# Performance work log

Hardware: AMD Instinct MI355X
Metric: run time of the kernel (lower is better)

The kernel has to match this reference:

```python
import jax, jax.numpy as jnp
import numpy as np

B, L, H, DK, DV, D, FC, NL = 8, 2016, 4, 32, 32, 256, 64, 3
EPS = 1e-5
SCALE = 1.0 / np.sqrt(float(D))  # module uses 1/sqrt(d_model), not 1/sqrt(dim_k)


def _ln(x, g, b):
    m = jnp.mean(x, axis=-1, keepdims=True)
    v = jnp.mean((x - m) ** 2, axis=-1, keepdims=True)
    return (x - m) * jax.lax.rsqrt(v + EPS) * g + b


def setup_inputs() -> dict:
    key = jax.random.key(0)
    ks = iter(jax.random.split(key, 32))

    def lin(k, shape, fan_in):
        # torch nn.Linear default: U(-1/sqrt(fan_in), 1/sqrt(fan_in))
        lim = 1.0 / np.sqrt(float(fan_in))
        return jax.random.uniform(k, shape, minval=-lim, maxval=lim, dtype=jnp.float32)

    inp = {
        'x': jax.random.normal(next(ks), (B, L, 2), dtype=jnp.float32),
        'in_w': lin(next(ks), (2, D), 2),
        'in_b': lin(next(ks), (D,), 2),
        'qw': lin(next(ks), (NL, D, H * DK), D),
        'qb': lin(next(ks), (NL, H * DK), D),
        'kw': lin(next(ks), (NL, D, H * DK), D),
        'kb': lin(next(ks), (NL, H * DK), D),
        'vw': lin(next(ks), (NL, D, H * DV), D),
        'vb': lin(next(ks), (NL, H * DV), D),
        'ow': lin(next(ks), (NL, H * DV, D), H * DV),
        'ob': lin(next(ks), (NL, D), H * DV),
        'f1w': lin(next(ks), (NL, D, FC), D),
        'f1b': lin(next(ks), (NL, FC), D),
        'f2w': lin(next(ks), (NL, FC, D), FC),
        'f2b': lin(next(ks), (NL, D), FC),
        'n1g': jnp.ones((NL, D), jnp.float32),
        'n1b': jnp.zeros((NL, D), jnp.float32),
        'n2g': jnp.ones((NL, D), jnp.float32),
        'n2b': jnp.zeros((NL, D), jnp.float32),
        'o1w': lin(next(ks), (D, D), D),
        'o1b': lin(next(ks), (D,), D),
        'o2w': lin(next(ks), (D, 2), D),
        'o2b': lin(next(ks), (2,), D),
    }
    return inp


def reference(x, in_w, in_b, qw, qb, kw, kb, vw, vb, ow, ob,
              f1w, f1b, f2w, f2b, n1g, n1b, n2g, n2b,
              o1w, o1b, o2w, o2b):
    h = x @ in_w + in_b  # (B, L, D)
    attns = []
    for i in range(NL):
        Q = (h @ qw[i] + qb[i]).reshape(B, L, H, DK)
        K = (h @ kw[i] + kb[i]).reshape(B, L, H, DK)
        V = (h @ vw[i] + vb[i]).reshape(B, L, H, DV)
        scores = jnp.einsum('blhe,bshe->bhls', Q, K) * SCALE  # (B,H,L,L)
        scores = jax.nn.softmax(scores, axis=-1)
        o = jnp.einsum('bhls,bshd->blhd', scores, V).reshape(B, L, H * DV)
        h = _ln(h + (o @ ow[i] + ob[i]), n1g[i], n1b[i])  # dropout is identity at eval
        ff = jax.nn.relu(h @ f1w[i] + f1b[i]) @ f2w[i] + f2b[i]
        h = _ln(h + ff, n2g[i], n2b[i])
        attns.append(scores)
    out = jax.nn.relu(h @ o1w + o1b) @ o2w + o2b  # (B, L, 2)
    return (out, jnp.stack(attns))
```

## Files before the change

kernel.cpp:

```cpp
#include <hip/hip_runtime.h>

typedef __attribute__((ext_vector_type(8))) short bh8;
typedef __attribute__((ext_vector_type(4))) float f32x4;

#define NB   8
#define NLAY 3
#define LSEQ 2016
#define NH   4
#define DM   256
#define FCN  64
#define MR   (NB*LSEQ)
#define SCL  0.0625f
#define SP   2024

__device__ __forceinline__ float b2f(unsigned short u) {
  union { unsigned int i; float f; } c; c.i = ((unsigned int)u) << 16; return c.f;
}
__device__ __forceinline__ unsigned short f2b(float f) {
  union { float f; unsigned int i; } c; c.f = f;
  unsigned int r = c.i + 0x7fffu + ((c.i >> 16) & 1u);
  return (unsigned short)(r >> 16);
}

__global__ __launch_bounds__(256) void k_f2bf(const float* __restrict__ s,
    unsigned short* __restrict__ d, int n) {
  int i = blockIdx.x * 256 + threadIdx.x;
  if (i < n) d[i] = f2b(s[i]);
}

__global__ __launch_bounds__(256) void k_embed(const float* __restrict__ x,
    const float* __restrict__ w, const float* __restrict__ bias,
    float* __restrict__ h, unsigned short* __restrict__ hb) {
  int m = blockIdx.x, d = threadIdx.x;
  float v = x[m*2] * w[d] + x[m*2+1] * w[DM + d] + bias[d];
  size_t idx = (size_t)m * DM + d;
  h[idx] = v;
  hb[idx] = f2b(v);
}

template<int MODE, int RELU>
__global__ __launch_bounds__(256) void k_gemm(
    const unsigned short* __restrict__ A, const unsigned short* __restrict__ W,
    const float* __restrict__ bias, const float* __restrict__ res,
    void* __restrict__ outp, int M, int N, int K)
{
  __shared__ unsigned short As[64 * 40];
  __shared__ unsigned short Ws[64 * 40];
  const int t = threadIdx.x;
  const int lane = t & 63, w = t >> 6;
  const int bm = blockIdx.y << 6, bn = blockIdx.x << 6;
  const int mw = (w & 1) << 5, nw = (w >> 1) << 5;
  const int q = lane >> 4, r = lane & 15;
  const int am = t >> 2, akc = (t & 3) << 3;
  const int wk = t >> 3, wnc = (t & 7) << 3;

  f32x4 zero = {0.f, 0.f, 0.f, 0.f};
  f32x4 acc[2][2] = {{zero, zero}, {zero, zero}};

  for (int k0 = 0; k0 < K; k0 += 32) {
    uint4 av = *(const uint4*)(A + (size_t)(bm + am) * K + k0 + akc);
    *(uint4*)(As + am * 40 + akc) = av;
    union { uint4 u; unsigned short s[8]; } wv;
    wv.u = *(const uint4*)(W + (size_t)(k0 + wk) * N + bn + wnc);
    #pragma unroll
    for (int j = 0; j < 8; ++j) Ws[(wnc + j) * 40 + wk] = wv.s[j];
    __syncthreads();

    bh8 a0 = *(const bh8*)(As + (mw + r) * 40 + (q << 3));
    bh8 a1 = *(const bh8*)(As + (mw + 16 + r) * 40 + (q << 3));
    bh8 b0 = *(const bh8*)(Ws + (nw + r) * 40 + (q << 3));
    bh8 b1 = *(const bh8*)(Ws + (nw + 16 + r) * 40 + (q << 3));
    acc[0][0] = __builtin_amdgcn_mfma_f32_16x16x32_bf16(a0, b0, acc[0][0], 0, 0, 0);
    acc[0][1] = __builtin_amdgcn_mfma_f32_16x16x32_bf16(a0, b1, acc[0][1], 0, 0, 0);
    acc[1][0] = __builtin_amdgcn_mfma_f32_16x16x32_bf16(a1, b0, acc[1][0], 0, 0, 0);
    acc[1][1] = __builtin_amdgcn_mfma_f32_16x16x32_bf16(a1, b1, acc[1][1], 0, 0, 0);
    __syncthreads();
  }

  #pragma unroll
  for (int mi = 0; mi < 2; ++mi)
  #pragma unroll
  for (int ni = 0; ni < 2; ++ni)
  #pragma unroll
  for (int rr = 0; rr < 4; ++rr) {
    int gm = bm + mw + (mi << 4) + (q << 2) + rr;
    int gn = bn + nw + (ni << 4) + r;
    float v = acc[mi][ni][rr] + bias[gn];
    if (RELU) v = v > 0.f ? v : 0.f;
    if (MODE == 0) {
      ((unsigned short*)outp)[(size_t)gm * N + gn] = f2b(v);
    } else if (MODE == 1) {
      int b = gm / LSEQ, l = gm - b * LSEQ;
      int hh = gn >> 5, e = gn & 31;
      ((unsigned short*)outp)[((((size_t)b * NH + hh) * LSEQ + l) << 5) + e] = f2b(v);
    } else if (MODE == 2) {
      int b = gm / LSEQ, l = gm - b * LSEQ;
      int hh = gn >> 5, e = gn & 31;
      ((unsigned short*)outp)[(((size_t)b * NH + hh) * 32 + e) * LSEQ + l] = f2b(v);
    } else {
      size_t idx = (size_t)gm * DM + gn;
      ((float*)outp)[idx] = v + res[idx];
    }
  }
}

__global__ __launch_bounds__(256) void k_ln(const float* __restrict__ y,
    const float* __restrict__ g, const float* __restrict__ bta,
    float* __restrict__ h, unsigned short* __restrict__ hb)
{
  int t = threadIdx.x, lane = t & 63, w = t >> 6;
  int row = blockIdx.x * 4 + w;
  const float* yr = y + (size_t)row * DM;
  float4 v = *(const float4*)(yr + lane * 4);
  float s = v.x + v.y + v.z + v.w;
  float sq = v.x * v.x + v.y * v.y + v.z * v.z + v.w * v.w;
  #pragma unroll
  for (int m = 1; m < 64; m <<= 1) { s += __shfl_xor(s, m, 64); sq += __shfl_xor(sq, m, 64); }
  float mean = s * (1.f / 256.f);
  float var = sq * (1.f / 256.f) - mean * mean;
  float rs = rsqrtf(var + 1e-5f);
  float4 gg = *(const float4*)(g + lane * 4);
  float4 bb = *(const float4*)(bta + lane * 4);
  float4 o;
  o.x = (v.x - mean) * rs * gg.x + bb.x;
  o.y = (v.y - mean) * rs * gg.y + bb.y;
  o.z = (v.z - mean) * rs * gg.z + bb.z;
  o.w = (v.w - mean) * rs * gg.w + bb.w;
  *(float4*)(h + (size_t)row * DM + lane * 4) = o;
  ushort4 u;
  u.x = f2b(o.x); u.y = f2b(o.y); u.z = f2b(o.z); u.w = f2b(o.w);
  *(ushort4*)(hb + (size_t)row * DM + lane * 4) = u;
}

__global__ __launch_bounds__(256) void k_attn(
    const unsigned short* __restrict__ Qb, const unsigned short* __restrict__ Kb,
    const unsigned short* __restrict__ Vt, float* __restrict__ Pout,
    unsigned short* __restrict__ ao)
{
  __shared__ unsigned short S[16 * SP];
  __shared__ float red[4 * 16 * 32];
  __shared__ float rinv[16];
  const int t = threadIdx.x, lane = t & 63, w = t >> 6;
  const int bid = blockIdx.x;
  const int rb = bid % 126, bh = bid / 126;
  const int l0 = rb << 4;
  const int q = lane >> 4, r = lane & 15;

  bh8 qf = *(const bh8*)(Qb + (((size_t)bh * LSEQ + l0 + r) << 5) + (q << 3));
  for (int st = w; st < 126; st += 4) {
    int s0 = st << 4;
    bh8 kf = *(const bh8*)(Kb + (((size_t)bh * LSEQ + s0 + r) << 5) + (q << 3));
    f32x4 c = {0.f, 0.f, 0.f, 0.f};
    c = __builtin_amdgcn_mfma_f32_16x16x32_bf16(qf, kf, c, 0, 0, 0);
    #pragma unroll
    for (int rr = 0; rr < 4; ++rr)
      S[(q * 4 + rr) * SP + s0 + r] = f2b(c[rr] * SCL);
  }
  __syncthreads();

  {
    int row = t >> 4, c = t & 15;
    float mx = -1e30f;
    for (int col = c; col < LSEQ; col += 16)
      mx = fmaxf(mx, b2f(S[row * SP + col]));
    #pragma unroll
    for (int m = 1; m < 16; m <<= 1) mx = fmaxf(mx, __shfl_xor(mx, m, 64));
    float sum = 0.f;
    for (int col = c; col < LSEQ; col += 16) {
      float e = __expf(b2f(S[row * SP + col]) - mx);
      sum += e;
      S[row * SP + col] = f2b(e);
    }
    #pragma unroll
    for (int m = 1; m < 16; m <<= 1) sum += __shfl_xor(sum, m, 64);
    if (c == 0) rinv[row] = 1.f / sum;
  }
  __syncthreads();

  float* prow0 = Pout + (size_t)bh * LSEQ * LSEQ + (size_t)l0 * LSEQ;
  for (int row = 0; row < 16; ++row) {
    float iv = rinv[row];
    float* pr = prow0 + (size_t)row * LSEQ;
    for (int col = t; col < LSEQ; col += 256)
      pr[col] = b2f(S[row * SP + col]) * iv;
  }

  f32x4 o0 = {0.f, 0.f, 0.f, 0.f}, o1 = {0.f, 0.f, 0.f, 0.f};
  const unsigned short* vtb = Vt + (size_t)bh * 32 * LSEQ;
  for (int st = w; st < 63; st += 4) {
    int s0 = st << 5;
    bh8 pf = *(const bh8*)(S + r * SP + s0 + (q << 3));
    bh8 v0 = *(const bh8*)(vtb + (size_t)r * LSEQ + s0 + (q << 3));
    bh8 v1 = *(const bh8*)(vtb + (size_t)(16 + r) * LSEQ + s0 + (q << 3));
    o0 = __builtin_amdgcn_mfma_f32_16x16x32_bf16(pf, v0, o0, 0, 0, 0);
    o1 = __builtin_amdgcn_mfma_f32_16x16x32_bf16(pf, v1, o1, 0, 0, 0);
  }
  float* rw = red + w * 512;
  #pragma unroll
  for (int rr = 0; rr < 4; ++rr) {
    rw[(q * 4 + rr) * 32 + r] = o0[rr];
    rw[(q * 4 + rr) * 32 + 16 + r] = o1[rr];
  }
  __syncthreads();
  for (int idx = t; idx < 512; idx += 256) {
    int row = idx >> 5, d = idx & 31;
    float v = red[idx] + red[512 + idx] + red[1024 + idx] + red[1536 + idx];
    v *= rinv[row];
    int b = bh >> 2, hh = bh & 3;
    ao[(size_t)(b * LSEQ + l0 + row) * 128 + (hh << 5) + d] = f2b(v);
  }
}

__global__ __launch_bounds__(256) void k_head(const unsigned short* __restrict__ t1,
    const float* __restrict__ o2w, const float* __restrict__ o2b,
    float* __restrict__ outp)
{
  int t = threadIdx.x, lane = t & 63, w = t >> 6;
  int row = blockIdx.x * 4 + w;
  union { ushort4 u; unsigned short s[4]; } pk;
  pk.u = *(const ushort4*)(t1 + (size_t)row * DM + lane * 4);
  float a0 = 0.f, a1 = 0.f;
  #pragma unroll
  for (int j = 0; j < 4; ++j) {
    float xv = b2f(pk.s[j]);
    int k = lane * 4 + j;
    a0 += xv * o2w[k * 2];
    a1 += xv * o2w[k * 2 + 1];
  }
  #pragma unroll
  for (int m = 1; m < 64; m <<= 1) { a0 += __shfl_xor(a0, m, 64); a1 += __shfl_xor(a1, m, 64); }
  if (lane == 0) {
    outp[(size_t)row * 2]     = a0 + o2b[0];
    outp[(size_t)row * 2 + 1] = a1 + o2b[1];
  }
}

extern "C" void kernel_launch(void* const* d_in, const int* in_sizes, int n_in,
                              void* d_out, int out_size, void* d_ws, size_t ws_size,
                              hipStream_t stream) {
  const float* x    = (const float*)d_in[0];
  const float* in_w = (const float*)d_in[1];
  const float* in_b = (const float*)d_in[2];
  const float* qw   = (const float*)d_in[3];
  const float* qb   = (const float*)d_in[4];
  const float* kw   = (const float*)d_in[5];
  const float* kb   = (const float*)d_in[6];
  const float* vw   = (const float*)d_in[7];
  const float* vb   = (const float*)d_in[8];
  const float* ow   = (const float*)d_in[9];
  const float* ob   = (const float*)d_in[10];
  const float* f1w  = (const float*)d_in[11];
  const float* f1b  = (const float*)d_in[12];
  const float* f2w  = (const float*)d_in[13];
  const float* f2b  = (const float*)d_in[14];
  const float* n1g  = (const float*)d_in[15];
  const float* n1b  = (const float*)d_in[16];
  const float* n2g  = (const float*)d_in[17];
  const float* n2b  = (const float*)d_in[18];
  const float* o1w  = (const float*)d_in[19];
  const float* o1b  = (const float*)d_in[20];
  const float* o2w  = (const float*)d_in[21];
  const float* o2b  = (const float*)d_in[22];

  char* p = (char*)d_ws;
  auto alloc = [&](size_t bytes) { char* r = p; p += (bytes + 255) & ~(size_t)255; return r; };
  float*          h    = (float*)alloc((size_t)MR * DM * 4);
  unsigned short* hb   = (unsigned short*)alloc((size_t)MR * DM * 2);
  float*          tmp  = (float*)alloc((size_t)MR * DM * 4);
  unsigned short* Qb   = (unsigned short*)alloc((size_t)MR * 128 * 2);
  unsigned short* Kb   = (unsigned short*)alloc((size_t)MR * 128 * 2);
  unsigned short* Vt   = (unsigned short*)alloc((size_t)MR * 128 * 2);
  unsigned short* ao   = (unsigned short*)alloc((size_t)MR * 128 * 2);
  unsigned short* Fb   = (unsigned short*)alloc((size_t)MR * FCN * 2);
  unsigned short* t1   = (unsigned short*)alloc((size_t)MR * DM * 2);
  unsigned short* qwb  = (unsigned short*)alloc(98304 * 2);
  unsigned short* kwb  = (unsigned short*)alloc(98304 * 2);
  unsigned short* vwb  = (unsigned short*)alloc(98304 * 2);
  unsigned short* owb  = (unsigned short*)alloc(98304 * 2);
  unsigned short* f1wb = (unsigned short*)alloc(49152 * 2);
  unsigned short* f2wb = (unsigned short*)alloc(49152 * 2);
  unsigned short* o1wb = (unsigned short*)alloc(65536 * 2);

  k_f2bf<<<(98304 + 255) / 256, 256, 0, stream>>>(qw, qwb, 98304);
  k_f2bf<<<(98304 + 255) / 256, 256, 0, stream>>>(kw, kwb, 98304);
  k_f2bf<<<(98304 + 255) / 256, 256, 0, stream>>>(vw, vwb, 98304);
  k_f2bf<<<(98304 + 255) / 256, 256, 0, stream>>>(ow, owb, 98304);
  k_f2bf<<<(49152 + 255) / 256, 256, 0, stream>>>(f1w, f1wb, 49152);
  k_f2bf<<<(49152 + 255) / 256, 256, 0, stream>>>(f2w, f2wb, 49152);
  k_f2bf<<<(65536 + 255) / 256, 256, 0, stream>>>(o1w, o1wb, 65536);

  k_embed<<<MR, 256, 0, stream>>>(x, in_w, in_b, h, hb);

  float* outp = (float*)d_out;
  for (int i = 0; i < NLAY; ++i) {
    k_gemm<1, 0><<<dim3(2, 252), 256, 0, stream>>>(hb, qwb + i * 32768, qb + i * 128, nullptr, Qb, MR, 128, 256);
    k_gemm<1, 0><<<dim3(2, 252), 256, 0, stream>>>(hb, kwb + i * 32768, kb + i * 128, nullptr, Kb, MR, 128, 256);
    k_gemm<2, 0><<<dim3(2, 252), 256, 0, stream>>>(hb, vwb + i * 32768, vb + i * 128, nullptr, Vt, MR, 128, 256);
    k_attn<<<4032, 256, 0, stream>>>(Qb, Kb, Vt,
        outp + 32256 + (size_t)i * NB * NH * LSEQ * LSEQ, ao);
    k_gemm<3, 0><<<dim3(4, 252), 256, 0, stream>>>(ao, owb + i * 32768, ob + i * 256, h, tmp, MR, 256, 128);
    k_ln<<<MR / 4, 256, 0, stream>>>(tmp, n1g + i * 256, n1b + i * 256, h, hb);
    k_gemm<0, 1><<<dim3(1, 252), 256, 0, stream>>>(hb, f1wb + i * 16384, f1b + i * 64, nullptr, Fb, MR, 64, 256);
    k_gemm<3, 0><<<dim3(4, 252), 256, 0, stream>>>(Fb, f2wb + i * 16384, f2b + i * 256, h, tmp, MR, 256, 64);
    k_ln<<<MR / 4, 256, 0, stream>>>(tmp, n2g + i * 256, n2b + i * 256, h, hb);
  }
  k_gemm<0, 1><<<dim3(4, 252), 256, 0, stream>>>(hb, o1wb, o1b, nullptr, t1, MR, 256, 256);
  k_head<<<MR / 4, 256, 0, stream>>>(t1, o2w, o2b, outp);
}
```

Before: 2.572 ms.

## Vectorize attention softmax/probability stores, fold scale into Q, prefetch GEMM tiles

The attention kernel now computes the transposed score tile (K·Qᵀ), so each lane writes packed bf16 pairs into shared memory. The softmax passes read 8 values per shared-memory access and write back through a hardware packed-convert instruction. The probability output uses float4 stores, and the P·V loop is unrolled by two over contiguous chunks per wave. The 1/sqrt(D) scale moves into the Q projection epilogue, the row stride is padded, and the padding is filled with a large negative value so the vector loops can cover full rows. The GEMM also register-prefetches the next K tile before the MFMAs. The intent is to cut shared-memory instruction count and widen the global stores of the large attention-probability tensor. The trade-offs are extra register pressure and rounding differences, since scaling now happens before the bf16 conversion of Q.

Result: faster. 2.139 ms (-16.8%).

```diff
diff --git a/kernel.cpp b/kernel.cpp
--- a/kernel.cpp
+++ b/kernel.cpp
@@ -11,7 +11,7 @@
 #define FCN  64
 #define MR   (NB*LSEQ)
 #define SCL  0.0625f
-#define SP   2024
+#define SP   2056
 
 __device__ __forceinline__ float b2f(unsigned short u) {
   union { unsigned int i; float f; } c; c.i = ((unsigned int)u) << 16; return c.f;
@@ -20,6 +20,11 @@
   union { float f; unsigned int i; } c; c.f = f;
   unsigned int r = c.i + 0x7fffu + ((c.i >> 16) & 1u);
   return (unsigned short)(r >> 16);
+}
+__device__ __forceinline__ unsigned int pk_bf16(float lo, float hi) {
+  unsigned int r;
+  asm("v_cvt_pk_bf16_f32 %0, %1, %2" : "=v"(r) : "v"(lo), "v"(hi));
+  return r;
 }
 
 __global__ __launch_bounds__(256) void k_f2bf(const float* __restrict__ s,
@@ -42,7 +47,7 @@
 __global__ __launch_bounds__(256) void k_gemm(
     const unsigned short* __restrict__ A, const unsigned short* __restrict__ W,
     const float* __restrict__ bias, const float* __restrict__ res,
-    void* __restrict__ outp, int M, int N, int K)
+    void* __restrict__ outp, float oscale, int M, int N, int K)
 {
   __shared__ unsigned short As[64 * 40];
   __shared__ unsigned short Ws[64 * 40];
@@ -57,14 +62,20 @@
   f32x4 zero = {0.f, 0.f, 0.f, 0.f};
   f32x4 acc[2][2] = {{zero, zero}, {zero, zero}};
 
+  uint4 av = *(const uint4*)(A + (size_t)(bm + am) * K + akc);
+  union { uint4 u; unsigned short s[8]; } wv;
+  wv.u = *(const uint4*)(W + (size_t)wk * N + bn + wnc);
+
   for (int k0 = 0; k0 < K; k0 += 32) {
-    uint4 av = *(const uint4*)(A + (size_t)(bm + am) * K + k0 + akc);
     *(uint4*)(As + am * 40 + akc) = av;
-    union { uint4 u; unsigned short s[8]; } wv;
-    wv.u = *(const uint4*)(W + (size_t)(k0 + wk) * N + bn + wnc);
     #pragma unroll
     for (int j = 0; j < 8; ++j) Ws[(wnc + j) * 40 + wk] = wv.s[j];
     __syncthreads();
+
+    if (k0 + 32 < K) {
+      av = *(const uint4*)(A + (size_t)(bm + am) * K + k0 + 32 + akc);
+      wv.u = *(const uint4*)(W + (size_t)(k0 + 32 + wk) * N + bn + wnc);
+    }
 
     bh8 a0 = *(const bh8*)(As + (mw + r) * 40 + (q << 3));
     bh8 a1 = *(const bh8*)(As + (mw + 16 + r) * 40 + (q << 3));
@@ -85,7 +96,7 @@
   for (int rr = 0; rr < 4; ++rr) {
     int gm = bm + mw + (mi << 4) + (q << 2) + rr;
     int gn = bn + nw + (ni << 4) + r;
-    float v = acc[mi][ni][rr] + bias[gn];
+    float v = (acc[mi][ni][rr] + bias[gn]) * oscale;
     if (RELU) v = v > 0.f ? v : 0.f;
     if (MODE == 0) {
       ((unsigned short*)outp)[(size_t)gm * N + gn] = f2b(v);
@@ -147,29 +158,55 @@
   const int q = lane >> 4, r = lane & 15;
 
   bh8 qf = *(const bh8*)(Qb + (((size_t)bh * LSEQ + l0 + r) << 5) + (q << 3));
-  for (int st = w; st < 126; st += 4) {
-    int s0 = st << 4;
-    bh8 kf = *(const bh8*)(Kb + (((size_t)bh * LSEQ + s0 + r) << 5) + (q << 3));
-    f32x4 c = {0.f, 0.f, 0.f, 0.f};
-    c = __builtin_amdgcn_mfma_f32_16x16x32_bf16(qf, kf, c, 0, 0, 0);
-    #pragma unroll
-    for (int rr = 0; rr < 4; ++rr)
-      S[(q * 4 + rr) * SP + s0 + r] = f2b(c[rr] * SCL);
-  }
+  {
+    const unsigned short* kb = Kb + (((size_t)bh * LSEQ) << 5) + (q << 3);
+    unsigned short* srow = S + r * SP;
+    int stb = w << 5;
+    int ste = (w == 3) ? 126 : stb + 32;
+    for (int st = stb; st < ste; st += 2) {
+      int s0 = st << 4, s1 = s0 + 16;
+      bh8 kf0 = *(const bh8*)(kb + ((size_t)(s0 + r) << 5));
+      bh8 kf1 = *(const bh8*)(kb + ((size_t)(s1 + r) << 5));
+      f32x4 c0 = {0.f,0.f,0.f,0.f}, c1 = {0.f,0.f,0.f,0.f};
+      c0 = __builtin_amdgcn_mfma_f32_16x16x32_bf16(kf0, qf, c0, 0, 0, 0);
+      c1 = __builtin_amdgcn_mfma_f32_16x16x32_bf16(kf1, qf, c1, 0, 0, 0);
+      uint2 u0, u1;
+      u0.x = pk_bf16(c0[0], c0[1]); u0.y = pk_bf16(c0[2], c0[3]);
+      u1.x = pk_bf16(c1[0], c1[1]); u1.y = pk_bf16(c1[2], c1[3]);
+      *(uint2*)(srow + s0 + (q << 2)) = u0;
+      *(uint2*)(srow + s1 + (q << 2)) = u1;
+    }
+  }
+  *(unsigned int*)(S + (t >> 4) * SP + 2016 + ((t & 15) << 1)) = 0xFF7FFF7Fu;
   __syncthreads();
 
   {
     int row = t >> 4, c = t & 15;
+    unsigned short* sr = S + row * SP;
     float mx = -1e30f;
-    for (int col = c; col < LSEQ; col += 16)
-      mx = fmaxf(mx, b2f(S[row * SP + col]));
+    #pragma unroll 4
+    for (int i = 0; i < 16; ++i) {
+      bh8 v = *(const bh8*)(sr + ((c + (i << 4)) << 3));
+      float m0 = fmaxf(fmaxf(b2f(v[0]), b2f(v[1])), fmaxf(b2f(v[2]), b2f(v[3])));
+      float m1 = fmaxf(fmaxf(b2f(v[4]), b2f(v[5])), fmaxf(b2f(v[6]), b2f(v[7])));
+      mx = fmaxf(mx, fmaxf(m0, m1));
+    }
     #pragma unroll
     for (int m = 1; m < 16; m <<= 1) mx = fmaxf(mx, __shfl_xor(mx, m, 64));
     float sum = 0.f;
-    for (int col = c; col < LSEQ; col += 16) {
-      float e = __expf(b2f(S[row * SP + col]) - mx);
-      sum += e;
-      S[row * SP + col] = f2b(e);
+    #pragma unroll 4
+    for (int i = 0; i < 16; ++i) {
+      unsigned short* sp = sr + ((c + (i << 4)) << 3);
+      bh8 v = *(const bh8*)sp;
+      float e0 = __expf(b2f(v[0]) - mx), e1 = __expf(b2f(v[1]) - mx);
+      float e2 = __expf(b2f(v[2]) - mx), e3 = __expf(b2f(v[3]) - mx);
+      float e4 = __expf(b2f(v[4]) - mx), e5 = __expf(b2f(v[5]) - mx);
+      float e6 = __expf(b2f(v[6]) - mx), e7 = __expf(b2f(v[7]) - mx);
+      sum += ((e0 + e1) + (e2 + e3)) + ((e4 + e5) + (e6 + e7));
+      uint4 pk;
+      pk.x = pk_bf16(e0, e1); pk.y = pk_bf16(e2, e3);
+      pk.z = pk_bf16(e4, e5); pk.w = pk_bf16(e6, e7);
+      *(uint4*)sp = pk;
     }
     #pragma unroll
     for (int m = 1; m < 16; m <<= 1) sum += __shfl_xor(sum, m, 64);
@@ -177,23 +214,51 @@
   }
   __syncthreads();
 
-  float* prow0 = Pout + (size_t)bh * LSEQ * LSEQ + (size_t)l0 * LSEQ;
-  for (int row = 0; row < 16; ++row) {
-    float iv = rinv[row];
-    float* pr = prow0 + (size_t)row * LSEQ;
-    for (int col = t; col < LSEQ; col += 256)
-      pr[col] = b2f(S[row * SP + col]) * iv;
+  {
+    float* prow0 = Pout + (size_t)bh * LSEQ * LSEQ + (size_t)l0 * LSEQ;
+    if (t < 252) {
+      for (int row = 0; row < 16; ++row) {
+        float iv = rinv[row];
+        bh8 v = *(const bh8*)(S + row * SP + (t << 3));
+        float4 o0, o1;
+        o0.x = b2f(v[0]) * iv; o0.y = b2f(v[1]) * iv;
+        o0.z = b2f(v[2]) * iv; o0.w = b2f(v[3]) * iv;
+        o1.x = b2f(v[4]) * iv; o1.y = b2f(v[5]) * iv;
+        o1.z = b2f(v[6]) * iv; o1.w = b2f(v[7]) * iv;
+        float* pr = prow0 + (size_t)row * LSEQ + (t << 3);
+        *(float4*)pr = o0;
+        *(float4*)(pr + 4) = o1;
+      }
+    }
   }
 
   f32x4 o0 = {0.f, 0.f, 0.f, 0.f}, o1 = {0.f, 0.f, 0.f, 0.f};
-  const unsigned short* vtb = Vt + (size_t)bh * 32 * LSEQ;
-  for (int st = w; st < 63; st += 4) {
-    int s0 = st << 5;
-    bh8 pf = *(const bh8*)(S + r * SP + s0 + (q << 3));
-    bh8 v0 = *(const bh8*)(vtb + (size_t)r * LSEQ + s0 + (q << 3));
-    bh8 v1 = *(const bh8*)(vtb + (size_t)(16 + r) * LSEQ + s0 + (q << 3));
-    o0 = __builtin_amdgcn_mfma_f32_16x16x32_bf16(pf, v0, o0, 0, 0, 0);
-    o1 = __builtin_amdgcn_mfma_f32_16x16x32_bf16(pf, v1, o1, 0, 0, 0);
+  {
+    const unsigned short* vtb = Vt + (size_t)bh * 32 * LSEQ + (q << 3);
+    const unsigned short* srow = S + r * SP + (q << 3);
+    int pb = w << 4;
+    int pe = (w == 3) ? 63 : pb + 16;
+    for (int st = pb; st + 1 < pe; st += 2) {
+      int s0 = st << 5, s1 = s0 + 32;
+      bh8 pf0 = *(const bh8*)(srow + s0);
+      bh8 pf1 = *(const bh8*)(srow + s1);
+      bh8 va0 = *(const bh8*)(vtb + (size_t)r * LSEQ + s0);
+      bh8 vb0 = *(const bh8*)(vtb + (size_t)(16 + r) * LSEQ + s0);
+      bh8 va1 = *(const bh8*)(vtb + (size_t)r * LSEQ + s1);
+      bh8 vb1 = *(const bh8*)(vtb + (size_t)(16 + r) * LSEQ + s1);
+      o0 = __builtin_amdgcn_mfma_f32_16x16x32_bf16(pf0, va0, o0, 0, 0, 0);
+      o1 = __builtin_amdgcn_mfma_f32_16x16x32_bf16(pf0, vb0, o1, 0, 0, 0);
+      o0 = __builtin_amdgcn_mfma_f32_16x16x32_bf16(pf1, va1, o0, 0, 0, 0);
+      o1 = __builtin_amdgcn_mfma_f32_16x16x32_bf16(pf1, vb1, o1, 0, 0, 0);
+    }
+    if ((pe - pb) & 1) {
+      int s0 = (pe - 1) << 5;
+      bh8 pf = *(const bh8*)(srow + s0);
+      bh8 va = *(const bh8*)(vtb + (size_t)r * LSEQ + s0);
+      bh8 vb = *(const bh8*)(vtb + (size_t)(16 + r) * LSEQ + s0);
+      o0 = __builtin_amdgcn_mfma_f32_16x16x32_bf16(pf, va, o0, 0, 0, 0);
+      o1 = __builtin_amdgcn_mfma_f32_16x16x32_bf16(pf, vb, o1, 0, 0, 0);
+    }
   }
   float* rw = red + w * 512;
   #pragma unroll
@@ -293,17 +358,17 @@
 
   float* outp = (float*)d_out;
   for (int i = 0; i < NLAY; ++i) {
-    k_gemm<1, 0><<<dim3(2, 252), 256, 0, stream>>>(hb, qwb + i * 32768, qb + i * 128, nullptr, Qb, MR, 128, 256);
-    k_gemm<1, 0><<<dim3(2, 252), 256, 0, stream>>>(hb, kwb + i * 32768, kb + i * 128, nullptr, Kb, MR, 128, 256);
-    k_gemm<2, 0><<<dim3(2, 252), 256, 0, stream>>>(hb, vwb + i * 32768, vb + i * 128, nullptr, Vt, MR, 128, 256);
+    k_gemm<1, 0><<<dim3(2, 252), 256, 0, stream>>>(hb, qwb + i * 32768, qb + i * 128, nullptr, Qb, SCL, MR, 128, 256);
+    k_gemm<1, 0><<<dim3(2, 252), 256, 0, stream>>>(hb, kwb + i * 32768, kb + i * 128, nullptr, Kb, 1.f, MR, 128, 256);
+    k_gemm<2, 0><<<dim3(2, 252), 256, 0, stream>>>(hb, vwb + i * 32768, vb + i * 128, nullptr, Vt, 1.f, MR, 128, 256);
     k_attn<<<4032, 256, 0, stream>>>(Qb, Kb, Vt,
         outp + 32256 + (size_t)i * NB * NH * LSEQ * LSEQ, ao);
-    k_gemm<3, 0><<<dim3(4, 252), 256, 0, stream>>>(ao, owb + i * 32768, ob + i * 256, h, tmp, MR, 256, 128);
+    k_gemm<3, 0><<<dim3(4, 252), 256, 0, stream>>>(ao, owb + i * 32768, ob + i * 256, h, tmp, 1.f, MR, 256, 128);
     k_ln<<<MR / 4, 256, 0, stream>>>(tmp, n1g + i * 256, n1b + i * 256, h, hb);
-    k_gemm<0, 1><<<dim3(1, 252), 256, 0, stream>>>(hb, f1wb + i * 16384, f1b + i * 64, nullptr, Fb, MR, 64, 256);
-    k_gemm<3, 0><<<dim3(4, 252), 256, 0, stream>>>(Fb, f2wb + i * 16384, f2b + i * 256, h, tmp, MR, 256, 64);
+    k_gemm<0, 1><<<dim3(1, 252), 256, 0, stream>>>(hb, f1wb + i * 16384, f1b + i * 64, nullptr, Fb, 1.f, MR, 64, 256);
+    k_gemm<3, 0><<<dim3(4, 252), 256, 0, stream>>>(Fb, f2wb + i * 16384, f2b + i * 256, h, tmp, 1.f, MR, 256, 64);
     k_ln<<<MR / 4, 256, 0, stream>>>(tmp, n2g + i * 256, n2b + i * 256, h, hb);
   }
-  k_gemm<0, 1><<<dim3(4, 252), 256, 0, stream>>>(hb, o1wb, o1b, nullptr, t1, MR, 256, 256);
+  k_gemm<0, 1><<<dim3(4, 252), 256, 0, stream>>>(hb, o1wb, o1b, nullptr, t1, 1.f, MR, 256, 256);
   k_head<<<MR / 4, 256, 0, stream>>>(t1, o2w, o2b, outp);
 }
```
